# Kernel tuning notes

Hardware: AMD Instinct MI355X
Metric: run time of the kernel (lower is better)

Reference implementation:

```python
import jax, jax.numpy as jnp
import numpy as np

N_HEAD, D_MODEL, D_HEAD = 16, 1024, 64
LN_EPS = 1e-5
SCALE = 1.0 / (D_HEAD ** 0.5)


def _rel_shift(x):
    # x: [qlen, klen, bsz, n_head]
    q, k, b, n = x.shape
    zero_pad = jnp.zeros((q, 1, b, n), x.dtype)
    x_padded = jnp.concatenate([zero_pad, x], axis=1)        # [q, k+1, b, n]
    x_padded = x_padded.reshape(k + 1, q, b, n)
    return x_padded[1:].reshape(q, k, b, n)


def setup_inputs() -> dict:
    key = jax.random.key(0)
    ks = jax.random.split(key, 8)
    qlen, bsz = 2048, 4
    H = N_HEAD * D_HEAD
    s = 0.02
    return {
        "w": jax.random.normal(ks[0], (qlen, bsz, D_MODEL), jnp.float32),
        "r": jax.random.normal(ks[1], (qlen, D_MODEL), jnp.float32),
        "qkv_w": jax.random.normal(ks[2], (3 * H, D_MODEL), jnp.float32) * s,
        "r_net_w": jax.random.normal(ks[3], (H, D_MODEL), jnp.float32) * s,
        "o_w": jax.random.normal(ks[4], (D_MODEL, H), jnp.float32) * s,
        "r_w_bias": jax.random.normal(ks[5], (N_HEAD, D_HEAD), jnp.float32) * s,
        "r_r_bias": jax.random.normal(ks[6], (N_HEAD, D_HEAD), jnp.float32) * s,
        "ln_g": jnp.ones((D_MODEL,), jnp.float32),
        "ln_b": jnp.zeros((D_MODEL,), jnp.float32),
    }


def _layer_norm(x, g, b):
    mu = jnp.mean(x, axis=-1, keepdims=True)
    var = jnp.var(x, axis=-1, keepdims=True)
    return (x - mu) * jax.lax.rsqrt(var + LN_EPS) * g + b


def reference(w, r, qkv_w, r_net_w, o_w, r_w_bias, r_r_bias, ln_g, ln_b):
    qlen, bsz, _ = w.shape
    rlen = r.shape[0]
    H = N_HEAD * D_HEAD

    w_heads = jnp.einsum('ibm,hm->ibh', w, qkv_w)            # [q,b,3H]
    r_head_k = jnp.einsum('jm,hm->jh', r, r_net_w)           # [r,H]

    w_head_q = w_heads[..., :H].reshape(qlen, bsz, N_HEAD, D_HEAD)
    w_head_k = w_heads[..., H:2 * H].reshape(qlen, bsz, N_HEAD, D_HEAD)
    w_head_v = w_heads[..., 2 * H:].reshape(qlen, bsz, N_HEAD, D_HEAD)
    r_head_k = r_head_k.reshape(rlen, N_HEAD, D_HEAD)

    AC = jnp.einsum('ibnd,jbnd->ijbn', w_head_q + r_w_bias, w_head_k)
    BD = jnp.einsum('ibnd,jnd->ijbn', w_head_q + r_r_bias, r_head_k)
    BD = _rel_shift(BD)

    attn_score = (AC + BD) * SCALE                           # [q,k,b,n]
    attn_prob = jax.nn.softmax(attn_score, axis=1)

    attn_vec = jnp.einsum('ijbn,jbnd->ibnd', attn_prob, w_head_v)
    attn_vec = attn_vec.reshape(qlen, bsz, H)
    attn_out = jnp.einsum('ibh,mh->ibm', attn_vec, o_w)

    return _layer_norm(w + attn_out, ln_g, ln_b)
```

## Files before the change

### kernel.cpp

```cpp
#include <hip/hip_runtime.h>
#include <hip/hip_bf16.h>
#include <stdint.h>

using bf16 = __hip_bfloat16;
typedef __attribute__((ext_vector_type(8))) short bf16x8;
typedef __attribute__((ext_vector_type(4))) float f32x4;

#define SCALE 0.125f

__device__ __forceinline__ float b2f(bf16 x) { return __bfloat162float(x); }
__device__ __forceinline__ bf16 f2b(float x) { return __float2bfloat16(x); }

__global__ __launch_bounds__(256) void cvt_kernel(const float* __restrict__ in, bf16* __restrict__ out, int n4) {
  int i = blockIdx.x * 256 + threadIdx.x;
  if (i >= n4) return;
  float4 v = ((const float4*)in)[i];
  alignas(8) bf16 o[4];
  o[0] = f2b(v.x); o[1] = f2b(v.y); o[2] = f2b(v.z); o[3] = f2b(v.w);
  ((uint2*)out)[i] = *(const uint2*)o;
}

template<int STORE_BF16>
__global__ __launch_bounds__(256) void gemm_bt(const bf16* __restrict__ A, const bf16* __restrict__ B,
                                               void* __restrict__ C, int M, int N, int K) {
  __shared__ bf16 As[128][72];
  __shared__ bf16 Bs[128][72];
  const int tid = threadIdx.x;
  const int lane = tid & 63;
  const int w = tid >> 6, wr = w >> 1, wc = w & 1;
  const int m0 = blockIdx.y * 128, n0 = blockIdx.x * 128;
  const int lr = lane & 15, lg = lane >> 4;
  f32x4 acc[4][4] = {};
  for (int k0 = 0; k0 < K; k0 += 64) {
    __syncthreads();
#pragma unroll
    for (int i = 0; i < 4; ++i) {
      int c = tid + i * 256;
      int row = c >> 3, seg = c & 7;
      *(int4*)&As[row][seg * 8] = *(const int4*)&A[(size_t)(m0 + row) * K + k0 + seg * 8];
      *(int4*)&Bs[row][seg * 8] = *(const int4*)&B[(size_t)(n0 + row) * K + k0 + seg * 8];
    }
    __syncthreads();
#pragma unroll
    for (int kk = 0; kk < 2; ++kk) {
      bf16x8 af[4], bfv[4];
#pragma unroll
      for (int m = 0; m < 4; ++m) af[m] = *(const bf16x8*)&As[wr * 64 + m * 16 + lr][kk * 32 + lg * 8];
#pragma unroll
      for (int n = 0; n < 4; ++n) bfv[n] = *(const bf16x8*)&Bs[wc * 64 + n * 16 + lr][kk * 32 + lg * 8];
#pragma unroll
      for (int m = 0; m < 4; ++m)
#pragma unroll
        for (int n = 0; n < 4; ++n)
          acc[m][n] = __builtin_amdgcn_mfma_f32_16x16x32_bf16(af[m], bfv[n], acc[m][n], 0, 0, 0);
    }
  }
#pragma unroll
  for (int m = 0; m < 4; ++m)
#pragma unroll
    for (int n = 0; n < 4; ++n)
#pragma unroll
      for (int r = 0; r < 4; ++r) {
        int row = m0 + wr * 64 + m * 16 + lg * 4 + r;
        int col = n0 + wc * 64 + n * 16 + lr;
        if (STORE_BF16) ((bf16*)C)[(size_t)row * N + col] = f2b(acc[m][n][r]);
        else            ((float*)C)[(size_t)row * N + col] = acc[m][n][r];
      }
}

__global__ __launch_bounds__(256) void flash_kernel(const bf16* __restrict__ wh, const bf16* __restrict__ rk,
                                                    const float* __restrict__ rwb, const float* __restrict__ rrb,
                                                    bf16* __restrict__ av) {
  const int bn = blockIdx.y;
  const int b = bn >> 4, n = bn & 15;
  const int q0 = blockIdx.x * 64;
  const int tid = threadIdx.x, lane = tid & 63, w = tid >> 6;
  const int lr = lane & 15, lg = lane >> 4;
  __shared__ bf16 Ks[64][64];
  __shared__ bf16 Vt[64][64];
  __shared__ bf16 Ps[64][64];
  __shared__ bf16 Tp[64][128];

  bf16x8 qf[2], qrf[2][2];
#pragma unroll
  for (int kk = 0; kk < 2; ++kk) {
    {
      int row = q0 + w * 16 + lr;
      int4 raw = *(const int4*)&wh[((size_t)row * 4 + b) * 3072 + n * 64 + kk * 32 + lg * 8];
      const bf16* rp = (const bf16*)&raw;
      alignas(16) bf16 ov[8];
#pragma unroll
      for (int e = 0; e < 8; ++e) ov[e] = f2b((b2f(rp[e]) + rwb[n * 64 + kk * 32 + lg * 8 + e]) * SCALE);
      qf[kk] = *(const bf16x8*)ov;
    }
#pragma unroll
    for (int ao = 0; ao < 2; ++ao) {
      int row = q0 + ao + w * 16 + lr; if (row > 2047) row = 2047;
      int4 raw = *(const int4*)&wh[((size_t)row * 4 + b) * 3072 + n * 64 + kk * 32 + lg * 8];
      const bf16* rp = (const bf16*)&raw;
      alignas(16) bf16 ov[8];
#pragma unroll
      for (int e = 0; e < 8; ++e) ov[e] = f2b((b2f(rp[e]) + rrb[n * 64 + kk * 32 + lg * 8 + e]) * SCALE);
      qrf[ao][kk] = *(const bf16x8*)ov;
    }
  }

  auto coords = [&](int u, int& pbase, int& sub) {
    int tt = 64 * u - q0;
    if (tt <= -64) { pbase = tt + 2048; sub = 0; } else { pbase = tt; sub = 2; }
  };

  auto panel_direct = [&](int pbase, int sub) {
    const int aidx = sub ? 1 : 0;
#pragma unroll
    for (int nt = 0; nt < 4; ++nt) {
      int c = pbase + nt * 16 + lr - sub;
      c = c < 0 ? 0 : (c > 2047 ? 2047 : c);
      f32x4 pacc = {};
      bf16x8 b0 = *(const bf16x8*)&rk[(size_t)c * 1024 + n * 64 + lg * 8];
      bf16x8 b1 = *(const bf16x8*)&rk[(size_t)c * 1024 + n * 64 + 32 + lg * 8];
      pacc = __builtin_amdgcn_mfma_f32_16x16x32_bf16(qrf[aidx][0], b0, pacc, 0, 0, 0);
      pacc = __builtin_amdgcn_mfma_f32_16x16x32_bf16(qrf[aidx][1], b1, pacc, 0, 0, 0);
      int cm = (pbase + nt * 16 + lr) & 127;
#pragma unroll
      for (int r = 0; r < 4; ++r) Tp[w * 16 + lg * 4 + r][cm] = f2b(pacc[r]);
    }
  };

  panel_direct(1984 - q0, 0);
  { int pb, sb; coords(0, pb, sb); panel_direct(pb, sb); }

  float mrow[4] = {-1e30f, -1e30f, -1e30f, -1e30f};
  float lrow[4] = {0.f, 0.f, 0.f, 0.f};
  f32x4 oacc[4] = {};

  for (int u = 0; u < 32; ++u) {
    const int j0 = u * 64;
    __syncthreads();
#pragma unroll
    for (int i = 0; i < 2; ++i) {
      int c = tid + i * 256;
      int row = c >> 3, seg = c & 7;
      int4 kv = *(const int4*)&wh[((size_t)(j0 + row) * 4 + b) * 3072 + 1024 + n * 64 + seg * 8];
      int4 vv = *(const int4*)&wh[((size_t)(j0 + row) * 4 + b) * 3072 + 2048 + n * 64 + seg * 8];
      *(int4*)&Ks[row][(seg ^ (row & 7)) * 8] = kv;
      const bf16* vp = (const bf16*)&vv;
#pragma unroll
      for (int e = 0; e < 8; ++e) {
        int d = seg * 8 + e;
        Vt[d][row ^ (((e ^ seg) & 7) << 3)] = vp[e];
      }
    }
    __syncthreads();

    f32x4 s[4] = {};
#pragma unroll
    for (int kk = 0; kk < 2; ++kk)
#pragma unroll
      for (int f = 0; f < 4; ++f) {
        int row = f * 16 + lr;
        bf16x8 kf = *(const bf16x8*)&Ks[row][((kk * 4 + lg) ^ (row & 7)) * 8];
        s[f] = __builtin_amdgcn_mfma_f32_16x16x32_bf16(qf[kk], kf, s[f], 0, 0, 0);
      }
#pragma unroll
    for (int f = 0; f < 4; ++f) {
      int jj = j0 + f * 16 + lr;
#pragma unroll
      for (int r = 0; r < 4; ++r) {
        int i = q0 + w * 16 + lg * 4 + r;
        int uu = jj - i;
        if (uu != 1) {
          int cm = (uu >= 2 ? uu : uu - 1) & 127;
          s[f][r] += b2f(Tp[w * 16 + lg * 4 + r][cm]);
        }
      }
    }
    float al[4];
#pragma unroll
    for (int r = 0; r < 4; ++r) {
      float mx = fmaxf(fmaxf(s[0][r], s[1][r]), fmaxf(s[2][r], s[3][r]));
#pragma unroll
      for (int msk = 1; msk <= 8; msk <<= 1) mx = fmaxf(mx, __shfl_xor(mx, msk));
      float mnew = fmaxf(mrow[r], mx);
      al[r] = __expf(mrow[r] - mnew);
      float rs = 0.f;
#pragma unroll
      for (int f = 0; f < 4; ++f) { float p = __expf(s[f][r] - mnew); s[f][r] = p; rs += p; }
#pragma unroll
      for (int msk = 1; msk <= 8; msk <<= 1) rs += __shfl_xor(rs, msk);
      lrow[r] = lrow[r] * al[r] + rs;
      mrow[r] = mnew;
    }
#pragma unroll
    for (int f = 0; f < 4; ++f)
#pragma unroll
      for (int r = 0; r < 4; ++r) {
        int row = w * 16 + lg * 4 + r;
        Ps[row][(f * 16 + lr) ^ ((row & 7) << 3)] = f2b(s[f][r]);
      }
#pragma unroll
    for (int df = 0; df < 4; ++df) {
      oacc[df][0] *= al[0]; oacc[df][1] *= al[1]; oacc[df][2] *= al[2]; oacc[df][3] *= al[3];
    }
#pragma unroll
    for (int kk = 0; kk < 2; ++kk) {
      bf16x8 pf = *(const bf16x8*)&Ps[w * 16 + lr][((kk * 4 + lg) ^ (lr & 7)) * 8];
#pragma unroll
      for (int df = 0; df < 4; ++df) {
        int d = df * 16 + lr;
        int vz = (d & 7) ^ ((d >> 3) & 7);
        bf16x8 vf = *(const bf16x8*)&Vt[d][((kk * 4 + lg) ^ vz) * 8];
        oacc[df] = __builtin_amdgcn_mfma_f32_16x16x32_bf16(pf, vf, oacc[df], 0, 0, 0);
      }
    }
    if (u < 31) {
      int pb, sb; coords(u + 1, pb, sb);
      panel_direct(pb, sb);
    }
  }
#pragma unroll
  for (int df = 0; df < 4; ++df)
#pragma unroll
    for (int r = 0; r < 4; ++r) {
      int i = q0 + w * 16 + lg * 4 + r;
      av[((size_t)i * 4 + b) * 1024 + n * 64 + df * 16 + lr] = f2b(oacc[df][r] / lrow[r]);
    }
}

__global__ __launch_bounds__(256) void ln_kernel(const float* __restrict__ w, const float* __restrict__ ao,
                                                 const float* __restrict__ g, const float* __restrict__ bb,
                                                 float* __restrict__ out) {
  const int row = blockIdx.x;
  const int t = threadIdx.x;
  const float4 wv = ((const float4*)(w + (size_t)row * 1024))[t];
  const float4 av = ((const float4*)(ao + (size_t)row * 1024))[t];
  float x0 = wv.x + av.x, x1 = wv.y + av.y, x2 = wv.z + av.z, x3 = wv.w + av.w;
  float s1 = x0 + x1 + x2 + x3;
  float s2 = x0 * x0 + x1 * x1 + x2 * x2 + x3 * x3;
#pragma unroll
  for (int m = 1; m <= 32; m <<= 1) { s1 += __shfl_xor(s1, m); s2 += __shfl_xor(s2, m); }
  __shared__ float red[8];
  const int lane = t & 63, wv2 = t >> 6;
  if (lane == 0) { red[wv2] = s1; red[4 + wv2] = s2; }
  __syncthreads();
  s1 = red[0] + red[1] + red[2] + red[3];
  s2 = red[4] + red[5] + red[6] + red[7];
  const float mu = s1 * (1.f / 1024.f);
  const float var = s2 * (1.f / 1024.f) - mu * mu;
  const float rr = rsqrtf(var + 1e-5f);
  const float4 gv = ((const float4*)g)[t];
  const float4 bv = ((const float4*)bb)[t];
  float4 o;
  o.x = (x0 - mu) * rr * gv.x + bv.x;
  o.y = (x1 - mu) * rr * gv.y + bv.y;
  o.z = (x2 - mu) * rr * gv.z + bv.z;
  o.w = (x3 - mu) * rr * gv.w + bv.w;
  ((float4*)(out + (size_t)row * 1024))[t] = o;
}

extern "C" void kernel_launch(void* const* d_in, const int* in_sizes, int n_in,
                              void* d_out, int out_size, void* d_ws, size_t ws_size,
                              hipStream_t stream) {
  const float* w    = (const float*)d_in[0];
  const float* r    = (const float*)d_in[1];
  const float* qkvw = (const float*)d_in[2];
  const float* rnw  = (const float*)d_in[3];
  const float* ow   = (const float*)d_in[4];
  const float* rwb  = (const float*)d_in[5];
  const float* rrb  = (const float*)d_in[6];
  const float* lng  = (const float*)d_in[7];
  const float* lnb  = (const float*)d_in[8];
  float* out = (float*)d_out;

  char* ws = (char*)d_ws;
  size_t off = 0;
  auto alloc = [&](size_t bytes) -> char* {
    char* p = ws + off; off += (bytes + 255) & ~((size_t)255); return p;
  };
  bf16*  wb  = (bf16*)alloc((size_t)8192 * 1024 * 2);
  bf16*  qb  = (bf16*)alloc((size_t)3072 * 1024 * 2);
  bf16*  rb  = (bf16*)alloc((size_t)2048 * 1024 * 2);
  bf16*  rnb = (bf16*)alloc((size_t)1024 * 1024 * 2);
  bf16*  owb = (bf16*)alloc((size_t)1024 * 1024 * 2);
  bf16*  wh  = (bf16*)alloc((size_t)8192 * 3072 * 2);
  bf16*  rkb = (bf16*)alloc((size_t)2048 * 1024 * 2);
  bf16*  avb = (bf16*)alloc((size_t)8192 * 1024 * 2);
  float* ao  = (float*)alloc((size_t)8192 * 1024 * 4);

  auto cvt = [&](const float* in, bf16* o, size_t nelem) {
    int n4 = (int)(nelem / 4);
    cvt_kernel<<<dim3((n4 + 255) / 256), dim3(256), 0, stream>>>(in, o, n4);
  };
  cvt(w, wb, (size_t)8192 * 1024);
  cvt(qkvw, qb, (size_t)3072 * 1024);
  cvt(r, rb, (size_t)2048 * 1024);
  cvt(rnw, rnb, (size_t)1024 * 1024);
  cvt(ow, owb, (size_t)1024 * 1024);

  gemm_bt<1><<<dim3(3072 / 128, 8192 / 128), dim3(256), 0, stream>>>(wb, qb, wh, 8192, 3072, 1024);
  gemm_bt<1><<<dim3(1024 / 128, 2048 / 128), dim3(256), 0, stream>>>(rb, rnb, rkb, 2048, 1024, 1024);

  flash_kernel<<<dim3(32, 64), dim3(256), 0, stream>>>(wh, rkb, rwb, rrb, avb);

  gemm_bt<0><<<dim3(1024 / 128, 8192 / 128), dim3(256), 0, stream>>>(avb, owb, ao, 8192, 1024, 1024);
  ln_kernel<<<dim3(8192), dim3(256), 0, stream>>>(w, ao, lng, lnb, out);
}
```

Before: 693.0 us.

## Double-buffer K/V via global_load_lds and read V with transpose LDS loads

The flash attention loop now prefetches the next K/V tile straight into a second LDS buffer with global_load_lds, so the copy overlaps compute of the current tile. V is no longer transposed element by element on store; it is laid out by the async load and read with ds_read_b64_tr_b16 transpose reads for the PV MFMA. One barrier per iteration replaces two. This removes the register staging and the scalar transposed LDS writes, at the cost of twice the K/V LDS and hand-written asm offsets that must match the layout exactly.

```diff
diff --git a/kernel.cpp b/kernel.cpp
--- a/kernel.cpp
+++ b/kernel.cpp
@@ -5,11 +5,22 @@
 using bf16 = __hip_bfloat16;
 typedef __attribute__((ext_vector_type(8))) short bf16x8;
 typedef __attribute__((ext_vector_type(4))) float f32x4;
+typedef __attribute__((ext_vector_type(2))) int i32x2;
 
 #define SCALE 0.125f
 
 __device__ __forceinline__ float b2f(bf16 x) { return __bfloat162float(x); }
 __device__ __forceinline__ bf16 f2b(float x) { return __float2bfloat16(x); }
+
+__device__ __forceinline__ void gll16(const void* g, void* l) {
+  __builtin_amdgcn_global_load_lds((const __attribute__((address_space(1))) void*)g,
+                                   (__attribute__((address_space(3))) void*)l, 16, 0, 0);
+}
+
+__device__ __forceinline__ bf16x8 cat64(i32x2 a, i32x2 b) {
+  int4 v; v.x = a.x; v.y = a.y; v.z = b.x; v.w = b.y;
+  return *(bf16x8*)&v;
+}
 
 __global__ __launch_bounds__(256) void cvt_kernel(const float* __restrict__ in, bf16* __restrict__ out, int n4) {
   int i = blockIdx.x * 256 + threadIdx.x;
@@ -76,8 +87,8 @@
   const int q0 = blockIdx.x * 64;
   const int tid = threadIdx.x, lane = tid & 63, w = tid >> 6;
   const int lr = lane & 15, lg = lane >> 4;
-  __shared__ bf16 Ks[64][64];
-  __shared__ bf16 Vt[64][64];
+  __shared__ bf16 Ks[2][64][64];
+  __shared__ bf16 VtA[2 * 4096];
   __shared__ bf16 Ps[64][64];
   __shared__ bf16 Tp[64][128];
 
@@ -127,31 +138,38 @@
     }
   };
 
+  auto stage = [&](int j0, int buf) {
+#pragma unroll
+    for (int i = 0; i < 2; ++i) {
+      int c = tid + i * 256;
+      int row = c >> 3, seg = c & 7;
+      int ss = seg ^ (row & 7);
+      gll16(&wh[((size_t)(j0 + row) * 4 + b) * 3072 + 1024 + n * 64 + ss * 8],
+            &Ks[buf][0][0] + (w * 64 + i * 256) * 8);
+      int jj = ((c >> 3) & 15) * 4 + ((c >> 1) & 3);
+      int d0 = (c >> 7) * 16 + (c & 1) * 8;
+      gll16(&wh[((size_t)(j0 + jj) * 4 + b) * 3072 + 2048 + n * 64 + d0],
+            &VtA[buf * 4096 + (w * 64 + i * 256) * 8]);
+    }
+  };
+
   panel_direct(1984 - q0, 0);
   { int pb, sb; coords(0, pb, sb); panel_direct(pb, sb); }
+  stage(0, 0);
+
+  const unsigned vtb = (unsigned)(uintptr_t)(__attribute__((address_space(3))) bf16*)VtA
+                       + (unsigned)(lg * 256 + lr * 2);
 
   float mrow[4] = {-1e30f, -1e30f, -1e30f, -1e30f};
   float lrow[4] = {0.f, 0.f, 0.f, 0.f};
   f32x4 oacc[4] = {};
 
+  __syncthreads();
+
+  int buf = 0;
   for (int u = 0; u < 32; ++u) {
     const int j0 = u * 64;
-    __syncthreads();
-#pragma unroll
-    for (int i = 0; i < 2; ++i) {
-      int c = tid + i * 256;
-      int row = c >> 3, seg = c & 7;
-      int4 kv = *(const int4*)&wh[((size_t)(j0 + row) * 4 + b) * 3072 + 1024 + n * 64 + seg * 8];
-      int4 vv = *(const int4*)&wh[((size_t)(j0 + row) * 4 + b) * 3072 + 2048 + n * 64 + seg * 8];
-      *(int4*)&Ks[row][(seg ^ (row & 7)) * 8] = kv;
-      const bf16* vp = (const bf16*)&vv;
-#pragma unroll
-      for (int e = 0; e < 8; ++e) {
-        int d = seg * 8 + e;
-        Vt[d][row ^ (((e ^ seg) & 7) << 3)] = vp[e];
-      }
-    }
-    __syncthreads();
+    if (u < 31) stage(j0 + 64, buf ^ 1);
 
     f32x4 s[4] = {};
 #pragma unroll
@@ -159,7 +177,7 @@
 #pragma unroll
       for (int f = 0; f < 4; ++f) {
         int row = f * 16 + lr;
-        bf16x8 kf = *(const bf16x8*)&Ks[row][((kk * 4 + lg) ^ (row & 7)) * 8];
+        bf16x8 kf = *(const bf16x8*)&Ks[buf][row][((kk * 4 + lg) ^ (row & 7)) * 8];
         s[f] = __builtin_amdgcn_mfma_f32_16x16x32_bf16(qf[kk], kf, s[f], 0, 0, 0);
       }
 #pragma unroll
@@ -202,21 +220,41 @@
     for (int df = 0; df < 4; ++df) {
       oacc[df][0] *= al[0]; oacc[df][1] *= al[1]; oacc[df][2] *= al[2]; oacc[df][3] *= al[3];
     }
-#pragma unroll
-    for (int kk = 0; kk < 2; ++kk) {
-      bf16x8 pf = *(const bf16x8*)&Ps[w * 16 + lr][((kk * 4 + lg) ^ (lr & 7)) * 8];
-#pragma unroll
-      for (int df = 0; df < 4; ++df) {
-        int d = df * 16 + lr;
-        int vz = (d & 7) ^ ((d >> 3) & 7);
-        bf16x8 vf = *(const bf16x8*)&Vt[d][((kk * 4 + lg) ^ vz) * 8];
-        oacc[df] = __builtin_amdgcn_mfma_f32_16x16x32_bf16(pf, vf, oacc[df], 0, 0, 0);
-      }
+    {
+      unsigned va = vtb + (unsigned)(buf << 13);
+      i32x2 t0, t1, t2, t3, t4, t5, t6, t7;
+      bf16x8 pf;
+#define TRRD(d_, o_) asm volatile("ds_read_b64_tr_b16 %0, %1 offset:" o_ : "=v"(d_) : "v"(va))
+      pf = *(const bf16x8*)&Ps[w * 16 + lr][((0 * 4 + lg) ^ (lr & 7)) * 8];
+      TRRD(t0, "0");    TRRD(t1, "128");
+      TRRD(t2, "2048"); TRRD(t3, "2176");
+      TRRD(t4, "4096"); TRRD(t5, "4224");
+      TRRD(t6, "6144"); TRRD(t7, "6272");
+      asm volatile("s_waitcnt lgkmcnt(0)" ::: "memory");
+      __builtin_amdgcn_sched_barrier(0);
+      oacc[0] = __builtin_amdgcn_mfma_f32_16x16x32_bf16(pf, cat64(t0, t1), oacc[0], 0, 0, 0);
+      oacc[1] = __builtin_amdgcn_mfma_f32_16x16x32_bf16(pf, cat64(t2, t3), oacc[1], 0, 0, 0);
+      oacc[2] = __builtin_amdgcn_mfma_f32_16x16x32_bf16(pf, cat64(t4, t5), oacc[2], 0, 0, 0);
+      oacc[3] = __builtin_amdgcn_mfma_f32_16x16x32_bf16(pf, cat64(t6, t7), oacc[3], 0, 0, 0);
+      pf = *(const bf16x8*)&Ps[w * 16 + lr][((1 * 4 + lg) ^ (lr & 7)) * 8];
+      TRRD(t0, "1024"); TRRD(t1, "1152");
+      TRRD(t2, "3072"); TRRD(t3, "3200");
+      TRRD(t4, "5120"); TRRD(t5, "5248");
+      TRRD(t6, "7168"); TRRD(t7, "7296");
+      asm volatile("s_waitcnt lgkmcnt(0)" ::: "memory");
+      __builtin_amdgcn_sched_barrier(0);
+      oacc[0] = __builtin_amdgcn_mfma_f32_16x16x32_bf16(pf, cat64(t0, t1), oacc[0], 0, 0, 0);
+      oacc[1] = __builtin_amdgcn_mfma_f32_16x16x32_bf16(pf, cat64(t2, t3), oacc[1], 0, 0, 0);
+      oacc[2] = __builtin_amdgcn_mfma_f32_16x16x32_bf16(pf, cat64(t4, t5), oacc[2], 0, 0, 0);
+      oacc[3] = __builtin_amdgcn_mfma_f32_16x16x32_bf16(pf, cat64(t6, t7), oacc[3], 0, 0, 0);
+#undef TRRD
     }
     if (u < 31) {
       int pb, sb; coords(u + 1, pb, sb);
       panel_direct(pb, sb);
     }
+    __syncthreads();
+    buf ^= 1;
   }
 #pragma unroll
   for (int df = 0; df < 4; ++df)
```

Measured after the change: 721.8 us. +4.1%, slower.
